# Kernel tuning notes

Hardware: AMD Instinct MI355X
Metric: run time of the kernel (lower is better)

## Reference

```python
import jax, jax.numpy as jnp
import numpy as np

EPS = 1e-9
TOP_K = 2


def setup_inputs() -> dict:
    key = jax.random.key(0)
    k = jax.random.split(key, 6)
    B, E, D_IN, D_MODEL, D_SEL = 16384, 8, 900, 512, 128
    return {
        "cycle_curve_data": jax.random.normal(k[0], (B, D_IN), jnp.float32),
        "logits": jax.random.normal(k[1], (B, E), jnp.float32),
        "moe_masks": jax.random.randint(k[2], (B, E), 0, 2, jnp.int32),
        "selection_embeddings": jax.random.normal(k[3], (B, E, D_SEL), jnp.float32),
        "W": jax.random.normal(k[4], (E, D_IN, D_MODEL), jnp.float32) / np.sqrt(D_IN).astype(np.float32),
        "b": jnp.zeros((E, D_MODEL), jnp.float32),
    }


def reference(cycle_curve_data, logits, moe_masks, selection_embeddings, W, b):
    B, E = logits.shape
    mask = (moe_masks == 1).astype(logits.dtype)  # [B, E]
    raw = jax.nn.softmax(logits, axis=1)          # [B, E]

    # inactive-expert mixture for selection embedding
    inactive = raw * (1.0 - mask)
    inactive = inactive / (jnp.sum(inactive, axis=1, keepdims=True) + EPS)
    selection_embedding = jnp.einsum("bes,be->bs", selection_embeddings, inactive)

    # active gates + top-k selection + renormalization
    active = raw * mask
    _, idx = jax.lax.top_k(active, TOP_K)                                  # [B, K]
    top_mask = jnp.sum(jax.nn.one_hot(idx, E, dtype=active.dtype), axis=1)  # [B, E]
    gates = active * top_mask
    gates = gates / (jnp.sum(gates, axis=1, keepdims=True) + EPS)

    # dense formulation of dispatch -> per-expert Linear -> weighted combine:
    # out[b] = sum_e gates[b,e] * (x[b] @ W[e] + b[e])
    expert_out = jnp.einsum("bd,edm->bem", cycle_curve_data, W) + b  # [B, E, D_model]
    final_out = jnp.einsum("bem,be->bm", expert_out, gates).astype(jnp.bfloat16)

    # guide loss (training-mode auxiliary loss)
    s = jnp.sum(raw * mask) / B
    guide_loss = (1.0 - s) * (1.0 - s)
    return final_out, guide_loss, selection_embedding
```

## Files before the change

kernel.cpp:

```cpp
#include <hip/hip_runtime.h>
#include <hip/hip_bf16.h>


#define B_ROWS 16384
#define DIN 900
#define DM 512
#define DSEL 128
#define KP 928
#define NKS 29
#define MAXT 192
#define EPSF 1e-9f

#define OUT_GUIDE (B_ROWS*DM)
#define OUT_SEL   (B_ROWS*DM + 1)

#define WS_COUNTS 0
#define WS_PART   512
#define WS_NT     768
#define WS_OFF    1024
#define WS_ENT    2048
#define WS_BB     9216
#define WS_PIDLR  25600
#define WS_GATEB  91136
#define WS_W8     222208
#define WS_ROWSS  746496
#define WS_WT     812032

typedef __attribute__((ext_vector_type(8))) short short8;
typedef __attribute__((ext_vector_type(8))) unsigned short ushort8;
typedef __attribute__((ext_vector_type(4))) float floatx4;

__device__ inline unsigned short f2bf(float v){
  union { __hip_bfloat16 h; unsigned short u; } c;
  c.h = __float2bfloat16(v);
  return c.u;
}
__device__ inline float bf2f(unsigned short u){
  union { unsigned int i; float f; } c;
  c.i = ((unsigned int)u) << 16;
  return c.f;
}
__device__ inline ushort8 pack8u(float4 a, float4 b){
  ushort8 c;
  c[0]=f2bf(a.x); c[1]=f2bf(a.y); c[2]=f2bf(a.z); c[3]=f2bf(a.w);
  c[4]=f2bf(b.x); c[5]=f2bf(b.y); c[6]=f2bf(b.z); c[7]=f2bf(b.w);
  return c;
}

__global__ __launch_bounds__(256) void prep_k(const float* __restrict__ W,
                                              unsigned short* __restrict__ wt2,
                                              const float* __restrict__ logits,
                                              const int* __restrict__ masks,
                                              float* __restrict__ partials,
                                              int* __restrict__ pidlr,
                                              float2* __restrict__ gatesb,
                                              float* __restrict__ w8,
                                              int* __restrict__ blockbase){
  __shared__ unsigned short lds[32][512];
  __shared__ int hist[64];
  __shared__ float wsum[4];
  int t = threadIdx.x;
  int bid = blockIdx.x;
  if (bid < 232){
    int kc = bid % 29, e = bid / 29;
    for (int kk = 0; kk < 32; ++kk){
      int k = kc*32 + kk;
      if (k < DIN){
        const float* wr = W + ((size_t)e*DIN + k)*DM;
        lds[kk][t]       = f2bf(wr[t]);
        lds[kk][t + 256] = f2bf(wr[t + 256]);
      } else {
        lds[kk][t] = 0; lds[kk][t + 256] = 0;
      }
    }
    __syncthreads();
    int ncg = t >> 3, q = t & 7;
    unsigned short* ob = wt2 + (((size_t)e*32 + ncg)*29 + kc)*512;
    for (int i = 0; i < 8; ++i){
      int fb = i*64 + q*8;
      int col = fb >> 5, kk0 = fb & 31;
      ushort8 y;
      #pragma unroll
      for (int j = 0; j < 8; ++j) y[j] = lds[kk0 + j][ncg*16 + col];
      *((ushort8*)(ob + fb)) = y;
    }
    return;
  }
  int gb = bid - 232;
  if (t < 64) hist[t] = 0;
  __syncthreads();
  int b = gb*256 + t;
  float4 l0 = *(const float4*)&logits[(size_t)b*8];
  float4 l1 = *(const float4*)&logits[(size_t)b*8 + 4];
  int4  m0 = *(const int4*)&masks[(size_t)b*8];
  int4  m1 = *(const int4*)&masks[(size_t)b*8 + 4];
  float raw[8] = {l0.x,l0.y,l0.z,l0.w,l1.x,l1.y,l1.z,l1.w};
  int   mk[8]  = {m0.x,m0.y,m0.z,m0.w,m1.x,m1.y,m1.z,m1.w};
  float mx = raw[0];
  for (int e = 1; e < 8; e++) mx = fmaxf(mx, raw[e]);
  float Z = 0.f;
  for (int e = 0; e < 8; e++){ raw[e] = expf(raw[e]-mx); Z += raw[e]; }
  float invZ = 1.f/Z;
  float act[8], ina[8]; float srm = 0.f, isum = 0.f;
  for (int e = 0; e < 8; e++){
    raw[e] *= invZ;
    if (mk[e] == 1){ act[e] = raw[e]; ina[e] = 0.f; srm += raw[e]; }
    else           { act[e] = 0.f;    ina[e] = raw[e]; isum += raw[e]; }
  }
  float v1 = -1.f, v2 = -1.f; int e1 = 0, e2 = 0;
  for (int e = 0; e < 8; e++){
    float a = act[e];
    if (a > v1){ v2 = v1; e2 = e1; v1 = a; e1 = e; }
    else if (a > v2){ v2 = a; e2 = e; }
  }
  float den = v1 + v2 + EPSF;
  float g1 = v1/den, g2 = v2/den;
  int lo, hi; float gl, gh;
  if (e1 < e2){ lo = e1; hi = e2; gl = g1; gh = g2; }
  else        { lo = e2; hi = e1; gl = g2; gh = g1; }
  int pid = lo*8 + hi;
  float invI = 1.f/(isum + EPSF);
  for (int e = 0; e < 8; e++) w8[(size_t)b*8 + e] = ina[e]*invI;
  gatesb[b] = make_float2(gl, gh);
  int lr = atomicAdd(&hist[pid], 1);
  pidlr[b] = pid | (lr << 8);
  float s = srm;
  for (int sft = 32; sft > 0; sft >>= 1) s += __shfl_down(s, sft, 64);
  if ((t & 63) == 0) wsum[t >> 6] = s;
  __syncthreads();
  if (t < 64) blockbase[gb*64 + t] = hist[t];
  if (t == 0) partials[gb] = wsum[0] + wsum[1] + wsum[2] + wsum[3];
}

__global__ void worklist_k(int* __restrict__ blockbase,
                           const float* __restrict__ partials,
                           int* __restrict__ off, int* __restrict__ ntp,
                           int4* __restrict__ entries,
                           float* __restrict__ out){
  int lane = threadIdx.x;
  int s = 0;
  for (int b0 = 0; b0 < 64; b0 += 16){
    int v[16];
    #pragma unroll
    for (int j = 0; j < 16; ++j) v[j] = blockbase[(b0+j)*64 + lane];
    #pragma unroll
    for (int j = 0; j < 16; ++j){ blockbase[(b0+j)*64 + lane] = s; s += v[j]; }
  }
  int c = s;
  int sc = c;
  for (int sh = 1; sh < 64; sh <<= 1){ int v = __shfl_up(sc, sh, 64); if (lane >= sh) sc += v; }
  int offp = sc - c;
  off[lane] = offp;
  int nt = (c + 127) >> 7;
  int snt = nt;
  for (int sh = 1; sh < 64; sh <<= 1){ int v = __shfl_up(snt, sh, 64); if (lane >= sh) snt += v; }
  int tbase = snt - nt;
  int elo = lane >> 3, ehi = lane & 7;
  for (int j = 0; j < nt; ++j){
    int nr = c - j*128; if (nr > 128) nr = 128;
    entries[tbase + j] = make_int4(elo, ehi, offp + j*128, nr);
  }
  int tot = __shfl(snt, 63, 64);
  if (lane == 0) *ntp = tot;
  float p = partials[lane];
  for (int sh = 32; sh > 0; sh >>= 1) p += __shfl_down(p, sh, 64);
  if (lane == 0){
    float sv = p * (1.f/B_ROWS);
    float d = 1.f - sv;
    out[OUT_GUIDE] = d*d;
  }
}

__global__ __launch_bounds__(256) void selemb_k(const float* __restrict__ sel,
                                                const float* __restrict__ w8,
                                                const int* __restrict__ pidlr,
                                                const int* __restrict__ off,
                                                const int* __restrict__ blockbase,
                                                int* __restrict__ rows_s,
                                                float* __restrict__ out){
  int t = threadIdx.x;
  int b = blockIdx.x*2 + (t >> 7);
  int d = t & 127;
  if (d == 0){
    int pl = pidlr[b];
    int p = pl & 63;
    int lr = pl >> 8;
    rows_s[off[p] + blockbase[(b >> 8)*64 + p] + lr] = b;
  }
  const float* wr = w8 + (size_t)b*8;
  const float* sb = sel + (size_t)b*(8*DSEL);
  float a = 0.f;
  for (int e = 0; e < 8; e++) a += wr[e] * sb[e*DSEL + d];
  out[OUT_SEL + (size_t)b*DSEL + d] = a;
}


#define ALOADV(P, kk) { \
  const float4* p_ = (const float4*)(xrow + (kk)*32); \
  P##0 = p_[0]; P##1 = p_[1]; P##2 = p_[2]; P##3 = p_[3]; }

#define ALOADT(P) { \
  float tmp[16]; \
  _Pragma("unroll") \
  for (int j = 0; j < 16; ++j){ \
    int k = 896 + skc*16 + j; \
    tmp[j] = (k < DIN) ? xrow[28*32 + j] : 0.f; \
  } \
  P##0 = make_float4(tmp[0],tmp[1],tmp[2],tmp[3]); \
  P##1 = make_float4(tmp[4],tmp[5],tmp[6],tmp[7]); \
  P##2 = make_float4(tmp[8],tmp[9],tmp[10],tmp[11]); \
  P##3 = make_float4(tmp[12],tmp[13],tmp[14],tmp[15]); }

#define AWR(buf, P) { \
  *((ushort8*)&as_[buf][srow*36 + skc*16])     = pack8u(P##0, P##1); \
  *((ushort8*)&as_[buf][srow*36 + skc*16 + 8]) = pack8u(P##2, P##3); }

#define BLOADG(kk) { \
  bw0 = *((const ushort8*)(bgp0 + (size_t)(kk)*512)); \
  bw1 = *((const ushort8*)(bgp1 + (size_t)(kk)*512)); \
  bw2 = *((const ushort8*)(bgp2 + (size_t)(kk)*512)); \
  bw3 = *((const ushort8*)(bgp3 + (size_t)(kk)*512)); }

#define BWR(buf) { \
  *((ushort8*)&bs_[buf][bo0]) = bw0; \
  *((ushort8*)&bs_[buf][bo1]) = bw1; \
  *((ushort8*)&bs_[buf][bo2]) = bw2; \
  *((ushort8*)&bs_[buf][bo3]) = bw3; }

#define KSTEP(cur) { \
  short8 af0 = *((const short8*)&as_[cur][(wrow*64 +  0 + l16)*36 + quad*8]); \
  short8 af1 = *((const short8*)&as_[cur][(wrow*64 + 16 + l16)*36 + quad*8]); \
  short8 af2 = *((const short8*)&as_[cur][(wrow*64 + 32 + l16)*36 + quad*8]); \
  short8 af3 = *((const short8*)&as_[cur][(wrow*64 + 48 + l16)*36 + quad*8]); \
  _Pragma("unroll") \
  for (int e = 0; e < 2; ++e){ \
    _Pragma("unroll") \
    for (int nt = 0; nt < 4; ++nt){ \
      short8 bfr = *((const short8*)&bs_[cur][(e*8 + wcol*4 + nt)*512 + quad*128 + l16*8]); \
      acc[e][0][nt] = __builtin_amdgcn_mfma_f32_16x16x32_bf16(af0, bfr, acc[e][0][nt], 0, 0, 0); \
      acc[e][1][nt] = __builtin_amdgcn_mfma_f32_16x16x32_bf16(af1, bfr, acc[e][1][nt], 0, 0, 0); \
      acc[e][2][nt] = __builtin_amdgcn_mfma_f32_16x16x32_bf16(af2, bfr, acc[e][2][nt], 0, 0, 0); \
      acc[e][3][nt] = __builtin_amdgcn_mfma_f32_16x16x32_bf16(af3, bfr, acc[e][3][nt], 0, 0, 0); \
    } \
  } }

__global__ __launch_bounds__(256, 2) void gemm_k(const float* __restrict__ xf,
                                                 const unsigned short* __restrict__ wt2,
                                                 const float* __restrict__ bias,
                                                 const int* __restrict__ ntp,
                                                 const int4* __restrict__ entries,
                                                 const int* __restrict__ rows_s,
                                                 const float2* __restrict__ gatesb,
                                                 float* __restrict__ out){
  int id = blockIdx.x;
  int tile = (id >> 5)*8 + (id & 7);
  int y = (id >> 3) & 3;
  if (tile >= *ntp) return;
  int4 ent = entries[tile];
  int elo = ent.x, ehi = ent.y, start = ent.z, nrows = ent.w;

  __shared__ __align__(16) unsigned short as_[2][128*36];
  __shared__ __align__(16) unsigned short bs_[2][16*512];
  __shared__ int   gidx_s[128];
  __shared__ float glo_s[128];
  __shared__ float ghi_s[128];

  int t = threadIdx.x;
  if (t < 128){
    if (t < nrows){
      int g = rows_s[start + t];
      gidx_s[t] = g;
      float2 gg = gatesb[g];
      glo_s[t] = gg.x; ghi_s[t] = gg.y;
    } else { gidx_s[t] = -1; glo_s[t] = 0.f; ghi_s[t] = 0.f; }
  }
  __syncthreads();

  int lane = t & 63, wid = t >> 6;
  int wrow = wid >> 1, wcol = wid & 1;
  int quad = lane >> 4, l16 = lane & 15;

  int srow = t >> 1, skc = t & 1;
  int sg = gidx_s[srow];
  const float* xrow = xf + (size_t)(sg >= 0 ? sg : 0)*DIN + skc*16;

  const unsigned short *bgp0, *bgp1, *bgp2, *bgp3;
  int bo0, bo1, bo2, bo3;
  {
    int v = t & 63;
    int goff = v*8;
    int lofs = (v & 3)*128 + (v >> 2)*8;
    int g0 = t >> 6, g1 = (256+t) >> 6, g2 = (512+t) >> 6, g3 = (768+t) >> 6;
    bgp0 = wt2 + ((size_t)((g0 < 8 ? elo : ehi)*32 + y*8 + (g0 & 7))*29)*512 + goff;
    bgp1 = wt2 + ((size_t)((g1 < 8 ? elo : ehi)*32 + y*8 + (g1 & 7))*29)*512 + goff;
    bgp2 = wt2 + ((size_t)((g2 < 8 ? elo : ehi)*32 + y*8 + (g2 & 7))*29)*512 + goff;
    bgp3 = wt2 + ((size_t)((g3 < 8 ? elo : ehi)*32 + y*8 + (g3 & 7))*29)*512 + goff;
    bo0 = g0*512 + lofs; bo1 = g1*512 + lofs; bo2 = g2*512 + lofs; bo3 = g3*512 + lofs;
  }

  floatx4 acc[2][4][4];
  #pragma unroll
  for (int i = 0; i < 2; i++)
    #pragma unroll
    for (int j = 0; j < 4; j++)
      #pragma unroll
      for (int k = 0; k < 4; k++)
        #pragma unroll
        for (int r = 0; r < 4; r++) acc[i][j][k][r] = 0.f;

  float4 rE0, rE1, rE2, rE3;
  float4 rO0, rO1, rO2, rO3;
  ushort8 bw0, bw1, bw2, bw3;

  ALOADV(rE, 0);
  ALOADV(rO, 1);
  BLOADG(0);
  AWR(0, rE); BWR(0);
  __syncthreads();

  for (int ks = 0; ks < 28; ks += 2){
    if (ks < 26){ ALOADV(rE, ks+2); } else { ALOADT(rE); }
    BLOADG(ks+1);
    KSTEP(0);
    AWR(1, rO); BWR(1);
    __syncthreads();
    if (ks < 26){ ALOADV(rO, ks+3); }
    BLOADG(ks+2);
    KSTEP(1);
    AWR(0, rE); BWR(0);
    __syncthreads();
  }
  KSTEP(0);

  int colbase = y*128 + wcol*64;
  float blo[4], bhi[4];
  #pragma unroll
  for (int nt = 0; nt < 4; ++nt){
    int n = colbase + nt*16 + l16;
    blo[nt] = bias[elo*DM + n];
    bhi[nt] = bias[ehi*DM + n];
  }
  #pragma unroll
  for (int mt = 0; mt < 4; ++mt){
    #pragma unroll
    for (int r = 0; r < 4; ++r){
      int rr = wrow*64 + mt*16 + quad*4 + r;
      int grow = gidx_s[rr];
      if (grow >= 0){
        float2 gg = gatesb[grow];
        float* orow = out + (size_t)grow*DM;
        #pragma unroll
        for (int nt = 0; nt < 4; ++nt){
          int n = colbase + nt*16 + l16;
          float v = gg.x*(acc[0][mt][nt][r] + blo[nt]) + gg.y*(acc[1][mt][nt][r] + bhi[nt]);
          orow[n] = bf2f(f2bf(v));
        }
      }
    }
  }
}

extern "C" void kernel_launch(void* const* d_in, const int* in_sizes, int n_in,
                              void* d_out, int out_size, void* d_ws, size_t ws_size,
                              hipStream_t stream){
  const float* x      = (const float*)d_in[0];
  const float* logits = (const float*)d_in[1];
  const int*   masks  = (const int*)d_in[2];
  const float* sel    = (const float*)d_in[3];
  const float* W      = (const float*)d_in[4];
  const float* bias   = (const float*)d_in[5];
  float* out = (float*)d_out;
  char* ws = (char*)d_ws;
  float*  partials = (float*)(ws + WS_PART);
  int*    ntp      = (int*)(ws + WS_NT);
  int*    off      = (int*)(ws + WS_OFF);
  int4*   entries  = (int4*)(ws + WS_ENT);
  int*    blockbase= (int*)(ws + WS_BB);
  int*    pidlr    = (int*)(ws + WS_PIDLR);
  float2* gatesb   = (float2*)(ws + WS_GATEB);
  float*  w8       = (float*)(ws + WS_W8);
  int*    rows_s   = (int*)(ws + WS_ROWSS);
  unsigned short* wt2 = (unsigned short*)(ws + WS_WT);

  prep_k<<<296, 256, 0, stream>>>(W, wt2, logits, masks, partials, pidlr, gatesb, w8, blockbase);
  worklist_k<<<1, 64, 0, stream>>>(blockbase, partials, off, ntp, entries, out);
  selemb_k<<<B_ROWS/2, 256, 0, stream>>>(sel, w8, pidlr, off, blockbase, rows_s, out);
  gemm_k<<<4*MAXT, 256, 0, stream>>>(x, wt2, bias, ntp, entries, rows_s, gatesb, out);
}
```

Before: 274.0 us.

## Group rows per single expert and combine expert outputs with atomic adds

Rows are now routed into eight per-expert groups instead of 64 expert-pair groups. Each GEMM tile computes only one expert's product, so it needs half the weight tiles in LDS, uses fewer accumulators and can run at higher occupancy. The two expert contributions per row are summed with float atomicAdd into a zero-initialised fp32 output, and a separate pass rounds the result to bf16. This is meant to cut padding waste and per-tile register and LDS pressure. In exchange it adds a memset, many global atomics and an extra full read/write pass over the output.

New measurement: 307.3 us. 12.1% more time.

```diff
diff --git a/kernel.cpp b/kernel.cpp
--- a/kernel.cpp
+++ b/kernel.cpp
@@ -8,13 +8,12 @@
 #define DSEL 128
 #define KP 928
 #define NKS 29
-#define MAXT 192
+#define MAXT_S 272
 #define EPSF 1e-9f
 
 #define OUT_GUIDE (B_ROWS*DM)
 #define OUT_SEL   (B_ROWS*DM + 1)
 
-#define WS_COUNTS 0
 #define WS_PART   512
 #define WS_NT     768
 #define WS_OFF    1024
@@ -24,7 +23,9 @@
 #define WS_GATEB  91136
 #define WS_W8     222208
 #define WS_ROWSS  746496
-#define WS_WT     812032
+#define WS_WT     877568
+
+#define FRSTRIDE 14848
 
 typedef __attribute__((ext_vector_type(8))) short short8;
 typedef __attribute__((ext_vector_type(8))) unsigned short ushort8;
@@ -57,7 +58,7 @@
                                               float* __restrict__ w8,
                                               int* __restrict__ blockbase){
   __shared__ unsigned short lds[32][512];
-  __shared__ int hist[64];
+  __shared__ int hist[8];
   __shared__ float wsum[4];
   int t = threadIdx.x;
   int bid = blockIdx.x;
@@ -87,7 +88,7 @@
     return;
   }
   int gb = bid - 232;
-  if (t < 64) hist[t] = 0;
+  if (t < 8) hist[t] = 0;
   __syncthreads();
   int b = gb*256 + t;
   float4 l0 = *(const float4*)&logits[(size_t)b*8];
@@ -118,17 +119,17 @@
   int lo, hi; float gl, gh;
   if (e1 < e2){ lo = e1; hi = e2; gl = g1; gh = g2; }
   else        { lo = e2; hi = e1; gl = g2; gh = g1; }
-  int pid = lo*8 + hi;
   float invI = 1.f/(isum + EPSF);
   for (int e = 0; e < 8; e++) w8[(size_t)b*8 + e] = ina[e]*invI;
   gatesb[b] = make_float2(gl, gh);
-  int lr = atomicAdd(&hist[pid], 1);
-  pidlr[b] = pid | (lr << 8);
+  int lrlo = atomicAdd(&hist[lo], 1);
+  int lrhi = atomicAdd(&hist[hi], 1);
+  pidlr[b] = (lo*8 + hi) | (lrlo << 6) | (lrhi << 14);
   float s = srm;
   for (int sft = 32; sft > 0; sft >>= 1) s += __shfl_down(s, sft, 64);
   if ((t & 63) == 0) wsum[t >> 6] = s;
   __syncthreads();
-  if (t < 64) blockbase[gb*64 + t] = hist[t];
+  if (t < 8) blockbase[gb*8 + t] = hist[t];
   if (t == 0) partials[gb] = wsum[0] + wsum[1] + wsum[2] + wsum[3];
 }
 
@@ -138,29 +139,33 @@
                            int4* __restrict__ entries,
                            float* __restrict__ out){
   int lane = threadIdx.x;
-  int s = 0;
-  for (int b0 = 0; b0 < 64; b0 += 16){
-    int v[16];
-    #pragma unroll
-    for (int j = 0; j < 16; ++j) v[j] = blockbase[(b0+j)*64 + lane];
-    #pragma unroll
-    for (int j = 0; j < 16; ++j){ blockbase[(b0+j)*64 + lane] = s; s += v[j]; }
-  }
-  int c = s;
-  int sc = c;
-  for (int sh = 1; sh < 64; sh <<= 1){ int v = __shfl_up(sc, sh, 64); if (lane >= sh) sc += v; }
-  int offp = sc - c;
-  off[lane] = offp;
-  int nt = (c + 127) >> 7;
-  int snt = nt;
-  for (int sh = 1; sh < 64; sh <<= 1){ int v = __shfl_up(snt, sh, 64); if (lane >= sh) snt += v; }
-  int tbase = snt - nt;
-  int elo = lane >> 3, ehi = lane & 7;
-  for (int j = 0; j < nt; ++j){
-    int nr = c - j*128; if (nr > 128) nr = 128;
-    entries[tbase + j] = make_int4(elo, ehi, offp + j*128, nr);
-  }
-  int tot = __shfl(snt, 63, 64);
+  int c = 0;
+  if (lane < 8){
+    int s = 0;
+    for (int b0 = 0; b0 < 64; b0 += 16){
+      int v[16];
+      #pragma unroll
+      for (int j = 0; j < 16; ++j) v[j] = blockbase[(b0+j)*8 + lane];
+      #pragma unroll
+      for (int j = 0; j < 16; ++j){ blockbase[(b0+j)*8 + lane] = s; s += v[j]; }
+    }
+    c = s;
+  }
+  int nt = (lane < 8) ? ((c + 127) >> 7) : 0;
+  int offp = 0, tbase = 0, tot = 0;
+  for (int j = 0; j < 8; ++j){
+    int cj  = __shfl(c, j, 64);
+    int ntj = __shfl(nt, j, 64);
+    if (j < lane){ offp += cj; tbase += ntj; }
+    tot += ntj;
+  }
+  if (lane < 8){
+    off[lane] = offp;
+    for (int j = 0; j < nt; ++j){
+      int nr = c - j*128; if (nr > 128) nr = 128;
+      entries[tbase + j] = make_int4(lane, 0, offp + j*128, nr);
+    }
+  }
   if (lane == 0) *ntp = tot;
   float p = partials[lane];
   for (int sh = 32; sh > 0; sh >>= 1) p += __shfl_down(p, sh, 64);
@@ -182,10 +187,13 @@
   int b = blockIdx.x*2 + (t >> 7);
   int d = t & 127;
   if (d == 0){
-    int pl = pidlr[b];
-    int p = pl & 63;
-    int lr = pl >> 8;
-    rows_s[off[p] + blockbase[(b >> 8)*64 + p] + lr] = b;
+    int v = pidlr[b];
+    int pid = v & 63;
+    int lo = pid >> 3, hi = pid & 7;
+    int lrlo = (v >> 6) & 255, lrhi = (v >> 14) & 255;
+    int gb = b >> 8;
+    rows_s[off[lo] + blockbase[gb*8 + lo] + lrlo] = b;
+    rows_s[off[hi] + blockbase[gb*8 + hi] + lrhi] = b;
   }
   const float* wr = w8 + (size_t)b*8;
   const float* sb = sel + (size_t)b*(8*DSEL);
@@ -212,58 +220,51 @@
   P##3 = make_float4(tmp[12],tmp[13],tmp[14],tmp[15]); }
 
 #define AWR(buf, P) { \
-  *((ushort8*)&as_[buf][srow*36 + skc*16])     = pack8u(P##0, P##1); \
-  *((ushort8*)&as_[buf][srow*36 + skc*16 + 8]) = pack8u(P##2, P##3); }
-
-#define BLOADG(kk) { \
-  bw0 = *((const ushort8*)(bgp0 + (size_t)(kk)*512)); \
-  bw1 = *((const ushort8*)(bgp1 + (size_t)(kk)*512)); \
-  bw2 = *((const ushort8*)(bgp2 + (size_t)(kk)*512)); \
-  bw3 = *((const ushort8*)(bgp3 + (size_t)(kk)*512)); }
-
-#define BWR(buf) { \
-  *((ushort8*)&bs_[buf][bo0]) = bw0; \
-  *((ushort8*)&bs_[buf][bo1]) = bw1; \
-  *((ushort8*)&bs_[buf][bo2]) = bw2; \
-  *((ushort8*)&bs_[buf][bo3]) = bw3; }
+  *((ushort8*)&as_[buf][srow*40 + skc*16])     = pack8u(P##0, P##1); \
+  *((ushort8*)&as_[buf][srow*40 + skc*16 + 8]) = pack8u(P##2, P##3); }
+
+#define BLOADG(P, kk) { \
+  P##0 = *((const ushort8*)(bgp0 + (size_t)(kk)*512)); \
+  P##1 = *((const ushort8*)(bgp1 + (size_t)(kk)*512)); }
+
+#define BWR(buf, P) { \
+  *((ushort8*)&bs_[buf][bo0]) = P##0; \
+  *((ushort8*)&bs_[buf][bo1]) = P##1; }
 
 #define KSTEP(cur) { \
-  short8 af0 = *((const short8*)&as_[cur][(wrow*64 +  0 + l16)*36 + quad*8]); \
-  short8 af1 = *((const short8*)&as_[cur][(wrow*64 + 16 + l16)*36 + quad*8]); \
-  short8 af2 = *((const short8*)&as_[cur][(wrow*64 + 32 + l16)*36 + quad*8]); \
-  short8 af3 = *((const short8*)&as_[cur][(wrow*64 + 48 + l16)*36 + quad*8]); \
+  short8 af0 = *((const short8*)&as_[cur][(wrow*64 +  0 + l16)*40 + quad*8]); \
+  short8 af1 = *((const short8*)&as_[cur][(wrow*64 + 16 + l16)*40 + quad*8]); \
+  short8 af2 = *((const short8*)&as_[cur][(wrow*64 + 32 + l16)*40 + quad*8]); \
+  short8 af3 = *((const short8*)&as_[cur][(wrow*64 + 48 + l16)*40 + quad*8]); \
   _Pragma("unroll") \
-  for (int e = 0; e < 2; ++e){ \
-    _Pragma("unroll") \
-    for (int nt = 0; nt < 4; ++nt){ \
-      short8 bfr = *((const short8*)&bs_[cur][(e*8 + wcol*4 + nt)*512 + quad*128 + l16*8]); \
-      acc[e][0][nt] = __builtin_amdgcn_mfma_f32_16x16x32_bf16(af0, bfr, acc[e][0][nt], 0, 0, 0); \
-      acc[e][1][nt] = __builtin_amdgcn_mfma_f32_16x16x32_bf16(af1, bfr, acc[e][1][nt], 0, 0, 0); \
-      acc[e][2][nt] = __builtin_amdgcn_mfma_f32_16x16x32_bf16(af2, bfr, acc[e][2][nt], 0, 0, 0); \
-      acc[e][3][nt] = __builtin_amdgcn_mfma_f32_16x16x32_bf16(af3, bfr, acc[e][3][nt], 0, 0, 0); \
-    } \
+  for (int nt = 0; nt < 4; ++nt){ \
+    short8 bfr = *((const short8*)&bs_[cur][(wcol*4 + nt)*512 + quad*128 + l16*8]); \
+    acc[0][nt] = __builtin_amdgcn_mfma_f32_16x16x32_bf16(af0, bfr, acc[0][nt], 0, 0, 0); \
+    acc[1][nt] = __builtin_amdgcn_mfma_f32_16x16x32_bf16(af1, bfr, acc[1][nt], 0, 0, 0); \
+    acc[2][nt] = __builtin_amdgcn_mfma_f32_16x16x32_bf16(af2, bfr, acc[2][nt], 0, 0, 0); \
+    acc[3][nt] = __builtin_amdgcn_mfma_f32_16x16x32_bf16(af3, bfr, acc[3][nt], 0, 0, 0); \
   } }
 
-__global__ __launch_bounds__(256, 2) void gemm_k(const float* __restrict__ xf,
+__global__ __launch_bounds__(256, 3) void gemm_k(const float* __restrict__ xf,
                                                  const unsigned short* __restrict__ wt2,
                                                  const float* __restrict__ bias,
                                                  const int* __restrict__ ntp,
                                                  const int4* __restrict__ entries,
                                                  const int* __restrict__ rows_s,
                                                  const float2* __restrict__ gatesb,
+                                                 const int* __restrict__ pidlr,
                                                  float* __restrict__ out){
   int id = blockIdx.x;
   int tile = (id >> 5)*8 + (id & 7);
   int y = (id >> 3) & 3;
   if (tile >= *ntp) return;
   int4 ent = entries[tile];
-  int elo = ent.x, ehi = ent.y, start = ent.z, nrows = ent.w;
-
-  __shared__ __align__(16) unsigned short as_[2][128*36];
-  __shared__ __align__(16) unsigned short bs_[2][16*512];
+  int e = ent.x, start = ent.z, nrows = ent.w;
+
+  __shared__ __align__(16) unsigned short as_[2][128*40];
+  __shared__ __align__(16) unsigned short bs_[2][8*512];
   __shared__ int   gidx_s[128];
-  __shared__ float glo_s[128];
-  __shared__ float ghi_s[128];
+  __shared__ float gate_s[128];
 
   int t = threadIdx.x;
   if (t < 128){
@@ -271,8 +272,9 @@
       int g = rows_s[start + t];
       gidx_s[t] = g;
       float2 gg = gatesb[g];
-      glo_s[t] = gg.x; ghi_s[t] = gg.y;
-    } else { gidx_s[t] = -1; glo_s[t] = 0.f; ghi_s[t] = 0.f; }
+      int lo = (pidlr[g] & 63) >> 3;
+      gate_s[t] = (e == lo) ? gg.x : gg.y;
+    } else { gidx_s[t] = -1; gate_s[t] = 0.f; }
   }
   __syncthreads();
 
@@ -284,62 +286,51 @@
   int sg = gidx_s[srow];
   const float* xrow = xf + (size_t)(sg >= 0 ? sg : 0)*DIN + skc*16;
 
-  const unsigned short *bgp0, *bgp1, *bgp2, *bgp3;
-  int bo0, bo1, bo2, bo3;
+  const unsigned short *bgp0, *bgp1;
+  int bo0, bo1;
   {
     int v = t & 63;
-    int goff = v*8;
     int lofs = (v & 3)*128 + (v >> 2)*8;
-    int g0 = t >> 6, g1 = (256+t) >> 6, g2 = (512+t) >> 6, g3 = (768+t) >> 6;
-    bgp0 = wt2 + ((size_t)((g0 < 8 ? elo : ehi)*32 + y*8 + (g0 & 7))*29)*512 + goff;
-    bgp1 = wt2 + ((size_t)((g1 < 8 ? elo : ehi)*32 + y*8 + (g1 & 7))*29)*512 + goff;
-    bgp2 = wt2 + ((size_t)((g2 < 8 ? elo : ehi)*32 + y*8 + (g2 & 7))*29)*512 + goff;
-    bgp3 = wt2 + ((size_t)((g3 < 8 ? elo : ehi)*32 + y*8 + (g3 & 7))*29)*512 + goff;
-    bo0 = g0*512 + lofs; bo1 = g1*512 + lofs; bo2 = g2*512 + lofs; bo3 = g3*512 + lofs;
-  }
-
-  floatx4 acc[2][4][4];
+    int g0 = t >> 6, g1 = (256 + t) >> 6;
+    bgp0 = wt2 + ((size_t)(e*32 + y*8 + g0))*FRSTRIDE + v*8;
+    bgp1 = wt2 + ((size_t)(e*32 + y*8 + g1))*FRSTRIDE + v*8;
+    bo0 = g0*512 + lofs; bo1 = g1*512 + lofs;
+  }
+
+  floatx4 acc[4][4];
   #pragma unroll
-  for (int i = 0; i < 2; i++)
+  for (int j = 0; j < 4; j++)
     #pragma unroll
-    for (int j = 0; j < 4; j++)
+    for (int k = 0; k < 4; k++)
       #pragma unroll
-      for (int k = 0; k < 4; k++)
-        #pragma unroll
-        for (int r = 0; r < 4; r++) acc[i][j][k][r] = 0.f;
+      for (int r = 0; r < 4; r++) acc[j][k][r] = 0.f;
 
   float4 rE0, rE1, rE2, rE3;
   float4 rO0, rO1, rO2, rO3;
-  ushort8 bw0, bw1, bw2, bw3;
-
-  ALOADV(rE, 0);
-  ALOADV(rO, 1);
-  BLOADG(0);
-  AWR(0, rE); BWR(0);
+  ushort8 bE0, bE1, bO0, bO1;
+
+  ALOADV(rE, 0); BLOADG(bE, 0);
+  ALOADV(rO, 1); BLOADG(bO, 1);
+  AWR(0, rE); BWR(0, bE);
   __syncthreads();
 
   for (int ks = 0; ks < 28; ks += 2){
     if (ks < 26){ ALOADV(rE, ks+2); } else { ALOADT(rE); }
-    BLOADG(ks+1);
+    BLOADG(bE, ks+2);
     KSTEP(0);
-    AWR(1, rO); BWR(1);
+    AWR(1, rO); BWR(1, bO);
     __syncthreads();
-    if (ks < 26){ ALOADV(rO, ks+3); }
-    BLOADG(ks+2);
+    if (ks < 26){ ALOADV(rO, ks+3); BLOADG(bO, ks+3); }
     KSTEP(1);
-    AWR(0, rE); BWR(0);
+    AWR(0, rE); BWR(0, bE);
     __syncthreads();
   }
   KSTEP(0);
 
   int colbase = y*128 + wcol*64;
-  float blo[4], bhi[4];
+  float be[4];
   #pragma unroll
-  for (int nt = 0; nt < 4; ++nt){
-    int n = colbase + nt*16 + l16;
-    blo[nt] = bias[elo*DM + n];
-    bhi[nt] = bias[ehi*DM + n];
-  }
+  for (int nt = 0; nt < 4; ++nt) be[nt] = bias[e*DM + colbase + nt*16 + l16];
   #pragma unroll
   for (int mt = 0; mt < 4; ++mt){
     #pragma unroll
@@ -347,16 +338,25 @@
       int rr = wrow*64 + mt*16 + quad*4 + r;
       int grow = gidx_s[rr];
       if (grow >= 0){
-        float2 gg = gatesb[grow];
-        float* orow = out + (size_t)grow*DM;
+        float g = gate_s[rr];
+        float* orow = out + (size_t)grow*DM + colbase;
         #pragma unroll
-        for (int nt = 0; nt < 4; ++nt){
-          int n = colbase + nt*16 + l16;
-          float v = gg.x*(acc[0][mt][nt][r] + blo[nt]) + gg.y*(acc[1][mt][nt][r] + bhi[nt]);
-          orow[n] = bf2f(f2bf(v));
-        }
+        for (int nt = 0; nt < 4; ++nt)
+          atomicAdd(orow + nt*16 + l16, g*(acc[mt][nt][r] + be[nt]));
       }
     }
+  }
+}
+
+__global__ __launch_bounds__(256) void round_k(float* __restrict__ out){
+  int base = blockIdx.x*1024 + threadIdx.x;
+  float4* p = (float4*)out;
+  #pragma unroll
+  for (int j = 0; j < 4; ++j){
+    float4 v = p[base + j*256];
+    v.x = bf2f(f2bf(v.x)); v.y = bf2f(f2bf(v.y));
+    v.z = bf2f(f2bf(v.z)); v.w = bf2f(f2bf(v.w));
+    p[base + j*256] = v;
   }
 }
 
@@ -382,8 +382,10 @@
   int*    rows_s   = (int*)(ws + WS_ROWSS);
   unsigned short* wt2 = (unsigned short*)(ws + WS_WT);
 
+  hipMemsetAsync(out, 0, (size_t)B_ROWS*DM*4, stream);
   prep_k<<<296, 256, 0, stream>>>(W, wt2, logits, masks, partials, pidlr, gatesb, w8, blockbase);
   worklist_k<<<1, 64, 0, stream>>>(blockbase, partials, off, ntp, entries, out);
   selemb_k<<<B_ROWS/2, 256, 0, stream>>>(sel, w8, pidlr, off, blockbase, rows_s, out);
-  gemm_k<<<4*MAXT, 256, 0, stream>>>(x, wt2, bias, ntp, entries, rows_s, gatesb, out);
-}
+  gemm_k<<<4*MAXT_S, 256, 0, stream>>>(x, wt2, bias, ntp, entries, rows_s, gatesb, pidlr, out);
+  round_k<<<B_ROWS*DM/4096, 256, 0, stream>>>(out);
+}
```
